# Kernel optimization log

Hardware: AMD Instinct MI355X
Metric: run time of the kernel (lower is better)

Reference implementation:

```python
import jax, jax.numpy as jnp
import numpy as np

N = 35709   # vertices
F = 70789   # triangles
B = 64
CAMERA_DISTANCE = 10.0
FOCAL = 1015.0
IMAGE_SIZE = 224

SH_A = (np.pi, 2 * np.pi / np.sqrt(3.0), 2 * np.pi / np.sqrt(8.0))
SH_C = (1 / np.sqrt(4 * np.pi), np.sqrt(3.0) / np.sqrt(4 * np.pi), 3 * np.sqrt(5.0) / np.sqrt(12 * np.pi))


def _persc_proj():
    center = IMAGE_SIZE / 2
    m = np.array([FOCAL, 0, center, 0, FOCAL, center, 0, 0, 1], dtype=np.float32).reshape(3, 3).T
    return jnp.asarray(m)


def setup_inputs() -> dict:
    key = jax.random.key(0)
    ks = jax.random.split(key, 9)
    return {
        "coeffs": jax.random.normal(ks[0], (B, 257), jnp.float32),
        "meanshape": jax.random.normal(ks[1], (3 * N,), jnp.float32),
        "idBase": jax.random.normal(ks[2], (3 * N, 80), jnp.float32),
        "exBase": jax.random.normal(ks[3], (3 * N, 64), jnp.float32),
        "meantex": jax.random.uniform(ks[4], (3 * N,), jnp.float32) * 255.0,
        "texBase": jax.random.normal(ks[5], (3 * N, 80), jnp.float32),
        "persc_proj": _persc_proj(),
        "init_lit": jnp.array([0.8, 0, 0, 0, 0, 0, 0, 0, 0], jnp.float32).reshape(1, 1, 9),
        "point_buf": jax.random.randint(ks[6], (N, 8), 0, F + 1),   # index F = zero-pad row
        "face_buf": jax.random.randint(ks[7], (F, 3), 0, N),
        "keypoints": jax.random.randint(ks[8], (68,), 0, N),
    }


def _l2norm(x):
    # matches torch F.normalize(p=2, eps=1e-12)
    return x / jnp.maximum(jnp.linalg.norm(x, axis=-1, keepdims=True), 1e-12)


def _rotation(angles):
    x, y, z = angles[:, 0], angles[:, 1], angles[:, 2]
    o, zr = jnp.ones_like(x), jnp.zeros_like(x)
    cx, sx = jnp.cos(x), jnp.sin(x)
    cy, sy = jnp.cos(y), jnp.sin(y)
    cz, sz = jnp.cos(z), jnp.sin(z)
    rx = jnp.stack([o, zr, zr, zr, cx, -sx, zr, sx, cx], -1).reshape(-1, 3, 3)
    ry = jnp.stack([cy, zr, sy, zr, o, zr, -sy, zr, cy], -1).reshape(-1, 3, 3)
    rz = jnp.stack([cz, -sz, zr, sz, cz, zr, zr, zr, o], -1).reshape(-1, 3, 3)
    return jnp.transpose(rz @ ry @ rx, (0, 2, 1))


def _compute_norm(face_shape, face_buf, point_buf):
    tri = face_shape[:, face_buf]                 # (B, F, 3verts, 3xyz) gather
    e1 = tri[:, :, 0] - tri[:, :, 1]
    e2 = tri[:, :, 1] - tri[:, :, 2]
    fn = _l2norm(jnp.cross(e1, e2))               # (B, F, 3)
    fn = jnp.concatenate([fn, jnp.zeros((fn.shape[0], 1, 3), fn.dtype)], axis=1)
    vn = jnp.sum(fn[:, point_buf], axis=2)        # (B, N, 3) gather-sum over 8 faces
    return _l2norm(vn)


def _compute_color(face_texture, face_norm, gamma, init_lit):
    a, c = SH_A, SH_C
    g = gamma.reshape(gamma.shape[0], 3, 9) + init_lit   # (B, 3, 9)
    g = jnp.transpose(g, (0, 2, 1))                      # (B, 9, 3)
    nx, ny, nz = face_norm[..., 0:1], face_norm[..., 1:2], face_norm[..., 2:3]
    Y = jnp.concatenate([
        a[0] * c[0] * jnp.ones_like(nx),
        -a[1] * c[1] * ny,
        a[1] * c[1] * nz,
        -a[1] * c[1] * nx,
        a[2] * c[2] * nx * ny,
        -a[2] * c[2] * ny * nz,
        0.5 * a[2] * c[2] / np.sqrt(3.0) * (3 * nz ** 2 - 1),
        -a[2] * c[2] * nx * nz,
        0.5 * a[2] * c[2] * (nx ** 2 - ny ** 2)], axis=-1)   # (B, N, 9)
    rgb = jnp.einsum('bnk,bkc->bnc', Y, g)
    return rgb * face_texture


def reference(coeffs, meanshape, idBase, exBase, meantex, texBase, persc_proj, init_lit, point_buf, face_buf, keypoints):
    id_c, ex_c, tex_c = coeffs[:, 0:80], coeffs[:, 80:144], coeffs[:, 144:224]
    angles, gamma, trans = coeffs[:, 224:227], coeffs[:, 227:254], coeffs[:, 254:257]
    Bsz = coeffs.shape[0]
    # shape blending (dense GEMMs)
    shape_flat = (jnp.einsum('ij,aj->ai', idBase, id_c)
                  + jnp.einsum('ij,aj->ai', exBase, ex_c)
                  + meanshape[None])
    face_shape = shape_flat.reshape(Bsz, -1, 3)
    rot = _rotation(angles)
    face_shape_t = face_shape @ rot + trans[:, None, :]
    # to camera: z -> camera_distance - z
    face_vertex = jnp.concatenate([face_shape_t[..., :2], CAMERA_DISTANCE - face_shape_t[..., 2:]], axis=-1)
    # perspective projection
    proj = face_vertex @ persc_proj
    face_proj = proj[..., :2] / proj[..., 2:]
    landmark = face_proj[:, keypoints, :]
    # texture blending
    face_texture = ((jnp.einsum('ij,aj->ai', texBase, tex_c) + meantex[None]) / 255.0).reshape(Bsz, -1, 3)
    # mesh normals on untransformed shape, rotated into camera frame
    face_norm = _compute_norm(face_shape, face_buf, point_buf)
    face_norm_r = face_norm @ rot
    face_color = _compute_color(face_texture, face_norm_r, gamma, init_lit)
    return face_vertex, face_color, landmark
```

## Files before the change

### kernel.cpp

```cpp
#include <hip/hip_runtime.h>

#define N_V 35709
#define N_F 70789
#define NR  (3*N_V)
#define NB  64

#define WS_ROT    0
#define WS_GM     576
#define WS_CTRS   2304
#define WS_CTRT   11520
#define WS_SHAPET 16640

__global__ __launch_bounds__(64) void k_setup_rot(
    const float* __restrict__ coeffs, const float* __restrict__ init_lit,
    float* __restrict__ rotM, float* __restrict__ gm)
{
    int b = threadIdx.x;
    const float* cb = coeffs + b * 257;

    float ax = cb[224], ay = cb[225], az = cb[226];
    float cx = cosf(ax), sx = sinf(ax);
    float cy = cosf(ay), sy = sinf(ay);
    float cz = cosf(az), sz = sinf(az);
    float m[9];
    m[0] = cz * cy;
    m[1] = cz * sy * sx - sz * cx;
    m[2] = sz * sx + cz * sy * cx;
    m[3] = sz * cy;
    m[4] = cz * cx + sz * sy * sx;
    m[5] = sz * sy * cx - cz * sx;
    m[6] = -sy;
    m[7] = cy * sx;
    m[8] = cy * cx;
#pragma unroll
    for (int k = 0; k < 9; k++) rotM[b * 9 + k] = m[k];

#pragma unroll
    for (int k = 0; k < 9; k++) {
        float il = init_lit[k];
#pragma unroll
        for (int c = 0; c < 3; c++)
            gm[b * 27 + k * 3 + c] = cb[227 + c * 9 + k] + il;
    }
}

__global__ __launch_bounds__(64) void k_transpose(
    const float* __restrict__ coeffs,
    float* __restrict__ ctrS, float* __restrict__ ctrT)
{
    int j = blockIdx.x;
    int b = threadIdx.x;
    float v = coeffs[b * 257 + j];
    if (j < 144) ctrS[j * 64 + b] = v;
    else         ctrT[(j - 144) * 64 + b] = v;
}

__global__ __launch_bounds__(256) void k_gemm_tile(
    const float* __restrict__ idBase, const float* __restrict__ exBase,
    const float* __restrict__ texBase, const float* __restrict__ meanshape,
    const float* __restrict__ meantex,
    const float* __restrict__ ctrS, const float* __restrict__ ctrT,
    float* __restrict__ shapeT,
    float* __restrict__ texT,
    int tex_transposed)
{
    __shared__ __align__(16) float As[16][68];
    __shared__ __align__(16) float Bs[16][64];

    const int t  = threadIdx.x;
    const int tn = t & 15;
    const int tm = t >> 4;
    const int r0 = blockIdx.x * 64;

    const int srow = t >> 2;
    const int sc   = t & 3;
    int srg = r0 + srow; if (srg > NR - 1) srg = NR - 1;

    float acc[4][4];

#pragma unroll
    for (int i = 0; i < 4; i++)
#pragma unroll
        for (int j = 0; j < 4; j++) acc[i][j] = 0.f;

    for (int kc = 0; kc < 9; kc++) {
        const float* src;
        int ld, k0;
        if (kc < 5) { src = idBase; ld = 80; k0 = kc * 16; }
        else        { src = exBase; ld = 64; k0 = (kc - 5) * 16; }

        {
            float4 v = *(const float4*)(src + (size_t)srg * ld + k0 + sc * 4);
            As[sc * 4 + 0][srow] = v.x;
            As[sc * 4 + 1][srow] = v.y;
            As[sc * 4 + 2][srow] = v.z;
            As[sc * 4 + 3][srow] = v.w;
        }
        ((float4*)&Bs[0][0])[t] = ((const float4*)(ctrS + (size_t)kc * 16 * 64))[t];
        __syncthreads();

#pragma unroll
        for (int k = 0; k < 16; k++) {
            float4 a = *(const float4*)&As[k][tm * 4];
            float4 b = *(const float4*)&Bs[k][tn * 4];
            float av[4] = {a.x, a.y, a.z, a.w};
            float bv[4] = {b.x, b.y, b.z, b.w};
#pragma unroll
            for (int i = 0; i < 4; i++)
#pragma unroll
                for (int j = 0; j < 4; j++)
                    acc[i][j] += av[i] * bv[j];
        }
        __syncthreads();
    }

#pragma unroll
    for (int i = 0; i < 4; i++) {
        int rg = r0 + tm * 4 + i;
        if (rg < NR) {
            float ms = meanshape[rg];
            float4 o = {acc[i][0] + ms, acc[i][1] + ms, acc[i][2] + ms, acc[i][3] + ms};
            *(float4*)(shapeT + (size_t)rg * 64 + tn * 4) = o;
        }
    }

#pragma unroll
    for (int i = 0; i < 4; i++)
#pragma unroll
        for (int j = 0; j < 4; j++) acc[i][j] = 0.f;

    for (int kc = 0; kc < 5; kc++) {
        int k0 = kc * 16;
        {
            float4 v = *(const float4*)(texBase + (size_t)srg * 80 + k0 + sc * 4);
            As[sc * 4 + 0][srow] = v.x;
            As[sc * 4 + 1][srow] = v.y;
            As[sc * 4 + 2][srow] = v.z;
            As[sc * 4 + 3][srow] = v.w;
        }
        ((float4*)&Bs[0][0])[t] = ((const float4*)(ctrT + (size_t)kc * 16 * 64))[t];
        __syncthreads();

#pragma unroll
        for (int k = 0; k < 16; k++) {
            float4 a = *(const float4*)&As[k][tm * 4];
            float4 b = *(const float4*)&Bs[k][tn * 4];
            float av[4] = {a.x, a.y, a.z, a.w};
            float bv[4] = {b.x, b.y, b.z, b.w};
#pragma unroll
            for (int i = 0; i < 4; i++)
#pragma unroll
                for (int j = 0; j < 4; j++)
                    acc[i][j] += av[i] * bv[j];
        }
        __syncthreads();
    }

    const float inv255 = 1.0f / 255.0f;
    if (tex_transposed) {
#pragma unroll
        for (int i = 0; i < 4; i++) {
            int rg = r0 + tm * 4 + i;
            if (rg < NR) {
                float mt = meantex[rg];
                float4 o = {(acc[i][0] + mt) * inv255, (acc[i][1] + mt) * inv255,
                            (acc[i][2] + mt) * inv255, (acc[i][3] + mt) * inv255};
                *(float4*)(texT + (size_t)rg * 64 + tn * 4) = o;
            }
        }
    } else {
#pragma unroll
        for (int i = 0; i < 4; i++) {
            int rg = r0 + tm * 4 + i;
            if (rg < NR) {
                float mt = meantex[rg];
#pragma unroll
                for (int j = 0; j < 4; j++)
                    texT[(size_t)(tn * 4 + j) * NR + rg] = (acc[i][j] + mt) * inv255;
            }
        }
    }
}

__global__ __launch_bounds__(256) void k_repack3(
    const float* __restrict__ shapeT, float* __restrict__ shape3)
{
    int wave = threadIdx.x >> 6;
    int b    = threadIdx.x & 63;
    int v0   = blockIdx.x * 32 + wave * 8;
#pragma unroll
    for (int r = 0; r < 8; r++) {
        int v = v0 + r;
        if (v < N_V) {
            float x = shapeT[(size_t)(3 * v)     * 64 + b];
            float y = shapeT[(size_t)(3 * v + 1) * 64 + b];
            float z = shapeT[(size_t)(3 * v + 2) * 64 + b];
            float* o = shape3 + ((size_t)v * 64 + b) * 3;
            o[0] = x; o[1] = y; o[2] = z;
        }
    }
}

__global__ __launch_bounds__(256) void k_facenorm3(
    const float* __restrict__ shape3,
    const int* __restrict__ face_buf,
    float* __restrict__ fnT3)
{
    int wave = threadIdx.x >> 6;
    int b    = threadIdx.x & 63;
    int f0   = blockIdx.x * 32 + wave * 8;
#pragma unroll
    for (int fr = 0; fr < 8; fr++) {
        int f = f0 + fr;
        if (f < N_F) {
            int i0 = face_buf[f * 3 + 0];
            int i1 = face_buf[f * 3 + 1];
            int i2 = face_buf[f * 3 + 2];
            const float* p0 = shape3 + ((size_t)i0 * 64 + b) * 3;
            const float* p1 = shape3 + ((size_t)i1 * 64 + b) * 3;
            const float* p2 = shape3 + ((size_t)i2 * 64 + b) * 3;
            float p0x = p0[0], p0y = p0[1], p0z = p0[2];
            float p1x = p1[0], p1y = p1[1], p1z = p1[2];
            float p2x = p2[0], p2y = p2[1], p2z = p2[2];
            float e1x = p0x - p1x, e1y = p0y - p1y, e1z = p0z - p1z;
            float e2x = p1x - p2x, e2y = p1y - p2y, e2z = p1z - p2z;
            float ccx = e1y * e2z - e1z * e2y;
            float ccy = e1z * e2x - e1x * e2z;
            float ccz = e1x * e2y - e1y * e2x;
            float l = sqrtf(ccx * ccx + ccy * ccy + ccz * ccz);
            float inv = 1.0f / fmaxf(l, 1e-12f);
            float* o = fnT3 + ((size_t)f * 64 + b) * 3;
            o[0] = ccx * inv; o[1] = ccy * inv; o[2] = ccz * inv;
        } else if (f == N_F) {
            float* o = fnT3 + ((size_t)f * 64 + b) * 3;
            o[0] = 0.f; o[1] = 0.f; o[2] = 0.f;
        }
    }
}

__global__ __launch_bounds__(256) void k_facenorm(
    const float* __restrict__ shapeT,
    const int* __restrict__ face_buf,
    float* __restrict__ fnT3)
{
    int wave = threadIdx.x >> 6;
    int b    = threadIdx.x & 63;
    int f0   = blockIdx.x * 32 + wave * 8;
#pragma unroll
    for (int fr = 0; fr < 8; fr++) {
        int f = f0 + fr;
        if (f < N_F) {
            int i0 = face_buf[f * 3 + 0];
            int i1 = face_buf[f * 3 + 1];
            int i2 = face_buf[f * 3 + 2];
            float p0x = shapeT[(size_t)(3 * i0)     * 64 + b];
            float p0y = shapeT[(size_t)(3 * i0 + 1) * 64 + b];
            float p0z = shapeT[(size_t)(3 * i0 + 2) * 64 + b];
            float p1x = shapeT[(size_t)(3 * i1)     * 64 + b];
            float p1y = shapeT[(size_t)(3 * i1 + 1) * 64 + b];
            float p1z = shapeT[(size_t)(3 * i1 + 2) * 64 + b];
            float p2x = shapeT[(size_t)(3 * i2)     * 64 + b];
            float p2y = shapeT[(size_t)(3 * i2 + 1) * 64 + b];
            float p2z = shapeT[(size_t)(3 * i2 + 2) * 64 + b];
            float e1x = p0x - p1x, e1y = p0y - p1y, e1z = p0z - p1z;
            float e2x = p1x - p2x, e2y = p1y - p2y, e2z = p1z - p2z;
            float ccx = e1y * e2z - e1z * e2y;
            float ccy = e1z * e2x - e1x * e2z;
            float ccz = e1x * e2y - e1y * e2x;
            float l = sqrtf(ccx * ccx + ccy * ccy + ccz * ccz);
            float inv = 1.0f / fmaxf(l, 1e-12f);
            float* o = fnT3 + ((size_t)f * 64 + b) * 3;
            o[0] = ccx * inv; o[1] = ccy * inv; o[2] = ccz * inv;
        } else if (f == N_F) {
            float* o = fnT3 + ((size_t)f * 64 + b) * 3;
            o[0] = 0.f; o[1] = 0.f; o[2] = 0.f;
        }
    }
}

__global__ __launch_bounds__(256) void k_vertex_fn(
    const float* __restrict__ shapeT,
    const float* __restrict__ texT,
    const float* __restrict__ fnT3,
    const float* __restrict__ rotM, const float* __restrict__ gm,
    const float* __restrict__ coeffs,
    const int* __restrict__ point_buf,
    float* __restrict__ out_vertex, float* __restrict__ out_color)
{
    __shared__ float sh[64 * 49];
    int wave = threadIdx.x >> 6;
    int b    = threadIdx.x & 63;
    int v0   = blockIdx.x * 16;
    int nvalid = N_V - v0; if (nvalid > 16) nvalid = 16;
    int kmax = 3 * nvalid;

    float m0 = rotM[b * 9 + 0], m1 = rotM[b * 9 + 1], m2 = rotM[b * 9 + 2];
    float m3 = rotM[b * 9 + 3], m4 = rotM[b * 9 + 4], m5 = rotM[b * 9 + 5];
    float m6 = rotM[b * 9 + 6], m7 = rotM[b * 9 + 7], m8 = rotM[b * 9 + 8];
    float tx = coeffs[b * 257 + 254], ty = coeffs[b * 257 + 255], tz = coeffs[b * 257 + 256];
    float g[27];
#pragma unroll
    for (int k = 0; k < 27; k++) g[k] = gm[b * 27 + k];

    const float A0C0 = 0.8862269254527580f;
    const float A1C1 = 1.7724538509055159f;
    const float A2C2 = 2.4270323912f;
    const float C6   = 0.7006239022f;
    const float C8   = 1.2135161956f;

    int pf[4][8];
    float sxv[4], syv[4], szv[4];
    float t0v[4], t1v[4], t2v[4];
#pragma unroll
    for (int vr = 0; vr < 4; vr++) {
        int v = v0 + wave * 4 + vr;
        int vc = (v < N_V) ? v : (N_V - 1);
#pragma unroll
        for (int k = 0; k < 8; k++) pf[vr][k] = point_buf[vc * 8 + k];
        sxv[vr] = shapeT[(size_t)(3 * vc)     * 64 + b];
        syv[vr] = shapeT[(size_t)(3 * vc + 1) * 64 + b];
        szv[vr] = shapeT[(size_t)(3 * vc + 2) * 64 + b];
        t0v[vr] = texT[(size_t)(3 * vc)     * 64 + b];
        t1v[vr] = texT[(size_t)(3 * vc + 1) * 64 + b];
        t2v[vr] = texT[(size_t)(3 * vc + 2) * 64 + b];
    }

    float vert[4][3];
    float col[4][3];

#pragma unroll
    for (int vr = 0; vr < 4; vr++) {
        float fx[8], fy[8], fz[8];
#pragma unroll
        for (int k = 0; k < 8; k++) {
            const float* fp = fnT3 + ((size_t)pf[vr][k] * 64 + b) * 3;
            fx[k] = fp[0]; fy[k] = fp[1]; fz[k] = fp[2];
        }

        float vx = m0 * sxv[vr] + m1 * syv[vr] + m2 * szv[vr] + tx;
        float vy = m3 * sxv[vr] + m4 * syv[vr] + m5 * szv[vr] + ty;
        float vz = m6 * sxv[vr] + m7 * syv[vr] + m8 * szv[vr] + tz;
        vert[vr][0] = vx; vert[vr][1] = vy; vert[vr][2] = 10.0f - vz;

        float nx = 0.f, ny = 0.f, nz = 0.f;
#pragma unroll
        for (int k = 0; k < 8; k++) { nx += fx[k]; ny += fy[k]; nz += fz[k]; }
        float l = sqrtf(nx * nx + ny * ny + nz * nz);
        float inv = 1.0f / fmaxf(l, 1e-12f);
        nx *= inv; ny *= inv; nz *= inv;

        float rx = m0 * nx + m1 * ny + m2 * nz;
        float ry = m3 * nx + m4 * ny + m5 * nz;
        float rz = m6 * nx + m7 * ny + m8 * nz;

        float Y0 = A0C0;
        float Y1 = -A1C1 * ry;
        float Y2 =  A1C1 * rz;
        float Y3 = -A1C1 * rx;
        float Y4 =  A2C2 * rx * ry;
        float Y5 = -A2C2 * ry * rz;
        float Y6 =  C6 * (3.f * rz * rz - 1.f);
        float Y7 = -A2C2 * rx * rz;
        float Y8 =  C8 * (rx * rx - ry * ry);

        float tex3[3] = {t0v[vr], t1v[vr], t2v[vr]};
#pragma unroll
        for (int c = 0; c < 3; c++) {
            float rgb = Y0 * g[0 + c] + Y1 * g[3 + c] + Y2 * g[6 + c] + Y3 * g[9 + c] +
                        Y4 * g[12 + c] + Y5 * g[15 + c] + Y6 * g[18 + c] + Y7 * g[21 + c] +
                        Y8 * g[24 + c];
            col[vr][c] = rgb * tex3[c];
        }
    }

#pragma unroll
    for (int vr = 0; vr < 4; vr++)
#pragma unroll
        for (int c = 0; c < 3; c++)
            sh[b * 49 + (wave * 4 + vr) * 3 + c] = vert[vr][c];
    __syncthreads();
#pragma unroll 4
    for (int it = 0; it < 12; it++) {
        int f = it * 256 + threadIdx.x;
        int bb = f / 48, k = f - bb * 48;
        if (k < kmax)
            __builtin_nontemporal_store(sh[bb * 49 + k],
                                        out_vertex + (size_t)bb * NR + 3 * (size_t)v0 + k);
    }
    __syncthreads();

#pragma unroll
    for (int vr = 0; vr < 4; vr++)
#pragma unroll
        for (int c = 0; c < 3; c++)
            sh[b * 49 + (wave * 4 + vr) * 3 + c] = col[vr][c];
    __syncthreads();
#pragma unroll 4
    for (int it = 0; it < 12; it++) {
        int f = it * 256 + threadIdx.x;
        int bb = f / 48, k = f - bb * 48;
        if (k < kmax)
            __builtin_nontemporal_store(sh[bb * 49 + k],
                                        out_color + (size_t)bb * NR + 3 * (size_t)v0 + k);
    }
}

__global__ __launch_bounds__(256) void k_vertex(
    const float* __restrict__ shapeT,
    const float* __restrict__ texT,
    const float* __restrict__ rotM, const float* __restrict__ gm,
    const float* __restrict__ coeffs,
    const int* __restrict__ point_buf, const int* __restrict__ face_buf,
    float* __restrict__ out_vertex, float* __restrict__ out_color,
    int tex_in_out)
{
    __shared__ float sh[64 * 97];
    int wave = threadIdx.x >> 6;
    int b    = threadIdx.x & 63;
    int v0   = blockIdx.x * 32;
    int nvalid = N_V - v0; if (nvalid > 32) nvalid = 32;
    int kmax = 3 * nvalid;

    float m0 = rotM[b * 9 + 0], m1 = rotM[b * 9 + 1], m2 = rotM[b * 9 + 2];
    float m3 = rotM[b * 9 + 3], m4 = rotM[b * 9 + 4], m5 = rotM[b * 9 + 5];
    float m6 = rotM[b * 9 + 6], m7 = rotM[b * 9 + 7], m8 = rotM[b * 9 + 8];
    float tx = coeffs[b * 257 + 254], ty = coeffs[b * 257 + 255], tz = coeffs[b * 257 + 256];
    float g[27];
#pragma unroll
    for (int k = 0; k < 27; k++) g[k] = gm[b * 27 + k];

    const float A0C0 = 0.8862269254527580f;
    const float A1C1 = 1.7724538509055159f;
    const float A2C2 = 2.4270323912f;
    const float C6   = 0.7006239022f;
    const float C8   = 1.2135161956f;

    float vert[8][3];
    float col[8][3];

#pragma unroll
    for (int vr = 0; vr < 8; vr++) {
        int v = v0 + wave * 8 + vr;
        bool valid = (v < N_V);
        int vc = valid ? v : (N_V - 1);

        float sx0 = shapeT[(size_t)(3 * vc)     * 64 + b];
        float sy0 = shapeT[(size_t)(3 * vc + 1) * 64 + b];
        float sz0 = shapeT[(size_t)(3 * vc + 2) * 64 + b];

        float vx = m0 * sx0 + m1 * sy0 + m2 * sz0 + tx;
        float vy = m3 * sx0 + m4 * sy0 + m5 * sz0 + ty;
        float vz = m6 * sx0 + m7 * sy0 + m8 * sz0 + tz;
        vert[vr][0] = vx; vert[vr][1] = vy; vert[vr][2] = 10.0f - vz;

        float nx = 0.f, ny = 0.f, nz = 0.f;
#pragma unroll
// ... 87 lines not shown
            __builtin_nontemporal_store(sh[bb * 97 + k],
                                        out_color + (size_t)bb * NR + 3 * (size_t)v0 + k);
    }
}

__global__ __launch_bounds__(64) void k_landmark(
    const float* __restrict__ shapeT, const int* __restrict__ keypoints,
    const float* __restrict__ rotM, const float* __restrict__ coeffs,
    const float* __restrict__ P,
    float* __restrict__ out_lm)
{
    int l = blockIdx.x;
    int b = threadIdx.x;
    int kp = keypoints[l];

    float m0 = rotM[b * 9 + 0], m1 = rotM[b * 9 + 1], m2 = rotM[b * 9 + 2];
    float m3 = rotM[b * 9 + 3], m4 = rotM[b * 9 + 4], m5 = rotM[b * 9 + 5];
    float m6 = rotM[b * 9 + 6], m7 = rotM[b * 9 + 7], m8 = rotM[b * 9 + 8];
    float tx = coeffs[b * 257 + 254], ty = coeffs[b * 257 + 255], tz = coeffs[b * 257 + 256];

    float sx0 = shapeT[(size_t)(3 * kp)     * 64 + b];
    float sy0 = shapeT[(size_t)(3 * kp + 1) * 64 + b];
    float sz0 = shapeT[(size_t)(3 * kp + 2) * 64 + b];

    float x = m0 * sx0 + m1 * sy0 + m2 * sz0 + tx;
    float y = m3 * sx0 + m4 * sy0 + m5 * sz0 + ty;
    float z = 10.0f - (m6 * sx0 + m7 * sy0 + m8 * sz0 + tz);

    float p0 = x * P[0] + y * P[3] + z * P[6];
    float p1 = x * P[1] + y * P[4] + z * P[7];
    float p2 = x * P[2] + y * P[5] + z * P[8];

    size_t o = ((size_t)b * 68 + l) * 2;
    out_lm[o]     = p0 / p2;
    out_lm[o + 1] = p1 / p2;
}

extern "C" void kernel_launch(void* const* d_in, const int* in_sizes, int n_in,
                              void* d_out, int out_size, void* d_ws, size_t ws_size,
                              hipStream_t stream) {
    const float* coeffs    = (const float*)d_in[0];
    const float* meanshape = (const float*)d_in[1];
    const float* idBase    = (const float*)d_in[2];
    const float* exBase    = (const float*)d_in[3];
    const float* meantex   = (const float*)d_in[4];
    const float* texBase   = (const float*)d_in[5];
    const float* persc     = (const float*)d_in[6];
    const float* init_lit  = (const float*)d_in[7];
    const int*   point_buf = (const int*)d_in[8];
    const int*   face_buf  = (const int*)d_in[9];
    const int*   keypoints = (const int*)d_in[10];

    float* ws = (float*)d_ws;
    float* rotM   = ws + WS_ROT;
    float* gm     = ws + WS_GM;
    float* ctrS   = ws + WS_CTRS;
    float* ctrT   = ws + WS_CTRT;
    float* shapeT = ws + WS_SHAPET;

    float* out_vertex = (float*)d_out;
    float* out_color  = out_vertex + (size_t)NB * NR;
    float* out_lm     = out_color  + (size_t)NB * NR;

    size_t NRx64   = (size_t)NR * 64;
    size_t fn3_len = (size_t)(N_F + 1) * 64 * 3;
    size_t sh3_len = (size_t)N_V * 64 * 3;

    size_t need_tex = ((size_t)WS_SHAPET + 2 * NRx64) * sizeof(float);
    size_t need_fn  = need_tex + fn3_len * sizeof(float);
    size_t need_s3  = need_fn + sh3_len * sizeof(float);

    int tex_transposed = (ws_size >= need_tex) ? 1 : 0;
    int use_fn         = (ws_size >= need_fn) ? 1 : 0;
    int use_s3         = (ws_size >= need_s3) ? 1 : 0;

    float* texT   = tex_transposed ? (shapeT + NRx64) : out_color;
    float* fnT3   = shapeT + 2 * NRx64;
    float* shape3 = fnT3 + fn3_len;

    k_setup_rot<<<1, 64, 0, stream>>>(coeffs, init_lit, rotM, gm);
    k_transpose<<<224, 64, 0, stream>>>(coeffs, ctrS, ctrT);

    int gb = (NR + 63) / 64;
    k_gemm_tile<<<gb, 256, 0, stream>>>(idBase, exBase, texBase, meanshape,
                                        meantex, ctrS, ctrT, shapeT, texT,
                                        tex_transposed);

    if (use_fn) {
        int fb = (N_F + 1 + 31) / 32;
        if (use_s3) {
            int rb = (N_V + 31) / 32;
            k_repack3<<<rb, 256, 0, stream>>>(shapeT, shape3);
            k_facenorm3<<<fb, 256, 0, stream>>>(shape3, face_buf, fnT3);
        } else {
            k_facenorm<<<fb, 256, 0, stream>>>(shapeT, face_buf, fnT3);
        }
        int vb = (N_V + 15) / 16;
        k_vertex_fn<<<vb, 256, 0, stream>>>(shapeT, texT, fnT3, rotM, gm, coeffs,
                                            point_buf, out_vertex, out_color);
    } else {
        int vb = (N_V + 31) / 32;
        k_vertex<<<vb, 256, 0, stream>>>(shapeT, tex_transposed ? texT : nullptr,
                                         rotM, gm, coeffs, point_buf, face_buf,
                                         out_vertex, out_color,
                                         tex_transposed ? 0 : 1);
    }

    k_landmark<<<68, 64, 0, stream>>>(shapeT, keypoints, rotM, coeffs, persc, out_lm);
}
```

Measured before the change: 278.6 us.

## Split shape/texture GEMMs, write vertex-major layout directly, co-schedule face normals

```diff
diff --git a/kernel.cpp b/kernel.cpp
--- a/kernel.cpp
+++ b/kernel.cpp
@@ -9,7 +9,7 @@
 #define WS_GM     576
 #define WS_CTRS   2304
 #define WS_CTRT   11520
-#define WS_SHAPET 16640
+#define WS_MAIN   16640
 
 __global__ __launch_bounds__(64) void k_setup_rot(
     const float* __restrict__ coeffs, const float* __restrict__ init_lit,
@@ -55,6 +55,332 @@
     else         ctrT[(j - 144) * 64 + b] = v;
 }
 
+__global__ __launch_bounds__(256) void k_gemm_shape3(
+    const float* __restrict__ idBase, const float* __restrict__ exBase,
+    const float* __restrict__ meanshape,
+    const float* __restrict__ ctrS,
+    float* __restrict__ shape3)
+{
+    __shared__ __align__(16) float As[16][68];
+    __shared__ __align__(16) float Bs[16][64];
+
+    const int t  = threadIdx.x;
+    const int tn = t & 15;
+    const int tm = t >> 4;
+    const int r0 = blockIdx.x * 64;
+
+    const int srow = t >> 2;
+    const int sc   = t & 3;
+    int srg = r0 + srow; if (srg > NR - 1) srg = NR - 1;
+
+    float acc[4][4];
+#pragma unroll
+    for (int i = 0; i < 4; i++)
+#pragma unroll
+        for (int j = 0; j < 4; j++) acc[i][j] = 0.f;
+
+    for (int kc = 0; kc < 9; kc++) {
+        const float* src;
+        int ld, k0;
+        if (kc < 5) { src = idBase; ld = 80; k0 = kc * 16; }
+        else        { src = exBase; ld = 64; k0 = (kc - 5) * 16; }
+
+        {
+            float4 v = *(const float4*)(src + (size_t)srg * ld + k0 + sc * 4);
+            As[sc * 4 + 0][srow] = v.x;
+            As[sc * 4 + 1][srow] = v.y;
+            As[sc * 4 + 2][srow] = v.z;
+            As[sc * 4 + 3][srow] = v.w;
+        }
+        ((float4*)&Bs[0][0])[t] = ((const float4*)(ctrS + (size_t)kc * 16 * 64))[t];
+        __syncthreads();
+
+#pragma unroll
+        for (int k = 0; k < 16; k++) {
+            float4 a = *(const float4*)&As[k][tm * 4];
+            float4 b = *(const float4*)&Bs[k][tn * 4];
+            float av[4] = {a.x, a.y, a.z, a.w};
+            float bv[4] = {b.x, b.y, b.z, b.w};
+#pragma unroll
+            for (int i = 0; i < 4; i++)
+#pragma unroll
+                for (int j = 0; j < 4; j++)
+                    acc[i][j] += av[i] * bv[j];
+        }
+        __syncthreads();
+    }
+
+#pragma unroll
+    for (int i = 0; i < 4; i++) {
+        int r = r0 + tm * 4 + i;
+        if (r < NR) {
+            float ms = meanshape[r];
+            int v = r / 3;
+            int c = r - v * 3;
+            float* o = shape3 + ((size_t)v * 64 + tn * 4) * 3 + c;
+            o[0] = acc[i][0] + ms;
+            o[3] = acc[i][1] + ms;
+            o[6] = acc[i][2] + ms;
+            o[9] = acc[i][3] + ms;
+        }
+    }
+}
+
+__global__ __launch_bounds__(256) void k_fn_texgemm(
+    const float* __restrict__ texBase, const float* __restrict__ meantex,
+    const float* __restrict__ ctrT,
+    const float* __restrict__ shape3, const int* __restrict__ face_buf,
+    float* __restrict__ tex3, float* __restrict__ fnT3, int GB)
+{
+    __shared__ __align__(16) float As[16][68];
+    __shared__ __align__(16) float Bs[16][64];
+
+    int x = blockIdx.x;
+    int role_tex, idx;
+    if (x < 2 * GB) { role_tex = ((x & 1) == 0); idx = x >> 1; }
+    else            { role_tex = 0; idx = x - GB; }
+
+    if (role_tex) {
+        const int t  = threadIdx.x;
+        const int tn = t & 15;
+        const int tm = t >> 4;
+        const int r0 = idx * 64;
+        const int srow = t >> 2;
+        const int sc   = t & 3;
+        int srg = r0 + srow; if (srg > NR - 1) srg = NR - 1;
+
+        float acc[4][4];
+#pragma unroll
+        for (int i = 0; i < 4; i++)
+#pragma unroll
+            for (int j = 0; j < 4; j++) acc[i][j] = 0.f;
+
+        for (int kc = 0; kc < 5; kc++) {
+            int k0 = kc * 16;
+            {
+                float4 v = *(const float4*)(texBase + (size_t)srg * 80 + k0 + sc * 4);
+                As[sc * 4 + 0][srow] = v.x;
+                As[sc * 4 + 1][srow] = v.y;
+                As[sc * 4 + 2][srow] = v.z;
+                As[sc * 4 + 3][srow] = v.w;
+            }
+            ((float4*)&Bs[0][0])[t] = ((const float4*)(ctrT + (size_t)kc * 16 * 64))[t];
+            __syncthreads();
+
+#pragma unroll
+            for (int k = 0; k < 16; k++) {
+                float4 a = *(const float4*)&As[k][tm * 4];
+                float4 b = *(const float4*)&Bs[k][tn * 4];
+                float av[4] = {a.x, a.y, a.z, a.w};
+                float bv[4] = {b.x, b.y, b.z, b.w};
+#pragma unroll
+                for (int i = 0; i < 4; i++)
+#pragma unroll
+                    for (int j = 0; j < 4; j++)
+                        acc[i][j] += av[i] * bv[j];
+            }
+            __syncthreads();
+        }
+
+        const float inv255 = 1.0f / 255.0f;
+#pragma unroll
+        for (int i = 0; i < 4; i++) {
+            int r = r0 + tm * 4 + i;
+            if (r < NR) {
+                float mt = meantex[r];
+                int v = r / 3;
+                int c = r - v * 3;
+                float* o = tex3 + ((size_t)v * 64 + tn * 4) * 3 + c;
+                o[0] = (acc[i][0] + mt) * inv255;
+                o[3] = (acc[i][1] + mt) * inv255;
+                o[6] = (acc[i][2] + mt) * inv255;
+                o[9] = (acc[i][3] + mt) * inv255;
+            }
+        }
+    } else {
+        int wave = threadIdx.x >> 6;
+        int b    = threadIdx.x & 63;
+        int f0   = idx * 32 + wave * 8;
+#pragma unroll
+        for (int fr = 0; fr < 8; fr++) {
+            int f = f0 + fr;
+            if (f < N_F) {
+                int i0 = face_buf[f * 3 + 0];
+                int i1 = face_buf[f * 3 + 1];
+                int i2 = face_buf[f * 3 + 2];
+                const float* p0 = shape3 + ((size_t)i0 * 64 + b) * 3;
+                const float* p1 = shape3 + ((size_t)i1 * 64 + b) * 3;
+                const float* p2 = shape3 + ((size_t)i2 * 64 + b) * 3;
+                float p0x = p0[0], p0y = p0[1], p0z = p0[2];
+                float p1x = p1[0], p1y = p1[1], p1z = p1[2];
+                float p2x = p2[0], p2y = p2[1], p2z = p2[2];
+                float e1x = p0x - p1x, e1y = p0y - p1y, e1z = p0z - p1z;
+                float e2x = p1x - p2x, e2y = p1y - p2y, e2z = p1z - p2z;
+                float ccx = e1y * e2z - e1z * e2y;
+                float ccy = e1z * e2x - e1x * e2z;
+                float ccz = e1x * e2y - e1y * e2x;
+                float l = sqrtf(ccx * ccx + ccy * ccy + ccz * ccz);
+                float inv = 1.0f / fmaxf(l, 1e-12f);
+                float* o = fnT3 + ((size_t)f * 64 + b) * 3;
+                o[0] = ccx * inv; o[1] = ccy * inv; o[2] = ccz * inv;
+            } else if (f == N_F) {
+                float* o = fnT3 + ((size_t)f * 64 + b) * 3;
+                o[0] = 0.f; o[1] = 0.f; o[2] = 0.f;
+            }
+        }
+    }
+}
+
+__global__ __launch_bounds__(256) void k_vertex_lm(
+    const float* __restrict__ shape3,
+    const float* __restrict__ tex3,
+    const float* __restrict__ fnT3,
+    const float* __restrict__ rotM, const float* __restrict__ gm,
+    const float* __restrict__ coeffs,
+    const int* __restrict__ point_buf, const int* __restrict__ keypoints,
+    const float* __restrict__ P,
+    float* __restrict__ out_vertex, float* __restrict__ out_color,
+    float* __restrict__ out_lm, int VB)
+{
+    __shared__ float sh[64 * 49];
+    int x    = blockIdx.x;
+    int wave = threadIdx.x >> 6;
+    int b    = threadIdx.x & 63;
+
+    float m0 = rotM[b * 9 + 0], m1 = rotM[b * 9 + 1], m2 = rotM[b * 9 + 2];
+    float m3 = rotM[b * 9 + 3], m4 = rotM[b * 9 + 4], m5 = rotM[b * 9 + 5];
+    float m6 = rotM[b * 9 + 6], m7 = rotM[b * 9 + 7], m8 = rotM[b * 9 + 8];
+    float tx = coeffs[b * 257 + 254], ty = coeffs[b * 257 + 255], tz = coeffs[b * 257 + 256];
+
+    if (x >= VB) {
+        int l = (x - VB) * 4 + wave;
+        if (l < 68) {
+            int kp = keypoints[l];
+            const float* sp = shape3 + ((size_t)kp * 64 + b) * 3;
+            float sx0 = sp[0], sy0 = sp[1], sz0 = sp[2];
+            float xx = m0 * sx0 + m1 * sy0 + m2 * sz0 + tx;
+            float yy = m3 * sx0 + m4 * sy0 + m5 * sz0 + ty;
+            float zz = 10.0f - (m6 * sx0 + m7 * sy0 + m8 * sz0 + tz);
+            float p0 = xx * P[0] + yy * P[3] + zz * P[6];
+            float p1 = xx * P[1] + yy * P[4] + zz * P[7];
+            float p2 = xx * P[2] + yy * P[5] + zz * P[8];
+            size_t o = ((size_t)b * 68 + l) * 2;
+            out_lm[o]     = p0 / p2;
+            out_lm[o + 1] = p1 / p2;
+        }
+        return;
+    }
+
+    int v0 = x * 16;
+    int nvalid = N_V - v0; if (nvalid > 16) nvalid = 16;
+    int kmax = 3 * nvalid;
+
+    float g[27];
+#pragma unroll
+    for (int k = 0; k < 27; k++) g[k] = gm[b * 27 + k];
+
+    const float A0C0 = 0.8862269254527580f;
+    const float A1C1 = 1.7724538509055159f;
+    const float A2C2 = 2.4270323912f;
+    const float C6   = 0.7006239022f;
+    const float C8   = 1.2135161956f;
+
+    int pf[4][8];
+    float sxv[4], syv[4], szv[4];
+    float t0v[4], t1v[4], t2v[4];
+#pragma unroll
+    for (int vr = 0; vr < 4; vr++) {
+        int v = v0 + wave * 4 + vr;
+        int vc = (v < N_V) ? v : (N_V - 1);
+#pragma unroll
+        for (int k = 0; k < 8; k++) pf[vr][k] = point_buf[vc * 8 + k];
+        const float* sp = shape3 + ((size_t)vc * 64 + b) * 3;
+        sxv[vr] = sp[0]; syv[vr] = sp[1]; szv[vr] = sp[2];
+        const float* tp = tex3 + ((size_t)vc * 64 + b) * 3;
+        t0v[vr] = tp[0]; t1v[vr] = tp[1]; t2v[vr] = tp[2];
+    }
+
+    float vert[4][3];
+    float col[4][3];
+
+#pragma unroll
+    for (int vr = 0; vr < 4; vr++) {
+        float fx[8], fy[8], fz[8];
+#pragma unroll
+        for (int k = 0; k < 8; k++) {
+            const float* fp = fnT3 + ((size_t)pf[vr][k] * 64 + b) * 3;
+            fx[k] = fp[0]; fy[k] = fp[1]; fz[k] = fp[2];
+        }
+
+        float vx = m0 * sxv[vr] + m1 * syv[vr] + m2 * szv[vr] + tx;
+        float vy = m3 * sxv[vr] + m4 * syv[vr] + m5 * szv[vr] + ty;
+        float vz = m6 * sxv[vr] + m7 * syv[vr] + m8 * szv[vr] + tz;
+        vert[vr][0] = vx; vert[vr][1] = vy; vert[vr][2] = 10.0f - vz;
+
+        float nx = 0.f, ny = 0.f, nz = 0.f;
+#pragma unroll
+        for (int k = 0; k < 8; k++) { nx += fx[k]; ny += fy[k]; nz += fz[k]; }
+        float l = sqrtf(nx * nx + ny * ny + nz * nz);
+        float inv = 1.0f / fmaxf(l, 1e-12f);
+        nx *= inv; ny *= inv; nz *= inv;
+
+        float rx = m0 * nx + m1 * ny + m2 * nz;
+        float ry = m3 * nx + m4 * ny + m5 * nz;
+        float rz = m6 * nx + m7 * ny + m8 * nz;
+
+        float Y0 = A0C0;
+        float Y1 = -A1C1 * ry;
+        float Y2 =  A1C1 * rz;
+        float Y3 = -A1C1 * rx;
+        float Y4 =  A2C2 * rx * ry;
+        float Y5 = -A2C2 * ry * rz;
+        float Y6 =  C6 * (3.f * rz * rz - 1.f);
+        float Y7 = -A2C2 * rx * rz;
+        float Y8 =  C8 * (rx * rx - ry * ry);
+
+        float tex3v[3] = {t0v[vr], t1v[vr], t2v[vr]};
+#pragma unroll
+        for (int c = 0; c < 3; c++) {
+            float rgb = Y0 * g[0 + c] + Y1 * g[3 + c] + Y2 * g[6 + c] + Y3 * g[9 + c] +
+                        Y4 * g[12 + c] + Y5 * g[15 + c] + Y6 * g[18 + c] + Y7 * g[21 + c] +
+                        Y8 * g[24 + c];
+            col[vr][c] = rgb * tex3v[c];
+        }
+    }
+
+#pragma unroll
+    for (int vr = 0; vr < 4; vr++)
+#pragma unroll
+        for (int c = 0; c < 3; c++)
+            sh[b * 49 + (wave * 4 + vr) * 3 + c] = vert[vr][c];
+    __syncthreads();
+#pragma unroll 4
+    for (int it = 0; it < 12; it++) {
+        int f = it * 256 + threadIdx.x;
+        int bb = f / 48, k = f - bb * 48;
+        if (k < kmax)
+            __builtin_nontemporal_store(sh[bb * 49 + k],
+                                        out_vertex + (size_t)bb * NR + 3 * (size_t)v0 + k);
+    }
+    __syncthreads();
+
+#pragma unroll
+    for (int vr = 0; vr < 4; vr++)
+#pragma unroll
+        for (int c = 0; c < 3; c++)
+            sh[b * 49 + (wave * 4 + vr) * 3 + c] = col[vr][c];
+    __syncthreads();
+#pragma unroll 4
+    for (int it = 0; it < 12; it++) {
+        int f = it * 256 + threadIdx.x;
+        int bb = f / 48, k = f - bb * 48;
+        if (k < kmax)
+            __builtin_nontemporal_store(sh[bb * 49 + k],
+                                        out_color + (size_t)bb * NR + 3 * (size_t)v0 + k);
+    }
+}
+
+
 __global__ __launch_bounds__(256) void k_gemm_tile(
     const float* __restrict__ idBase, const float* __restrict__ exBase,
     const float* __restrict__ texBase, const float* __restrict__ meanshape,
@@ -77,7 +403,6 @@
     int srg = r0 + srow; if (srg > NR - 1) srg = NR - 1;
 
     float acc[4][4];
-
 #pragma unroll
     for (int i = 0; i < 4; i++)
 #pragma unroll
@@ -88,7 +413,6 @@
         int ld, k0;
         if (kc < 5) { src = idBase; ld = 80; k0 = kc * 16; }
         else        { src = exBase; ld = 64; k0 = (kc - 5) * 16; }
-
         {
             float4 v = *(const float4*)(src + (size_t)srg * ld + k0 + sc * 4);
             As[sc * 4 + 0][srow] = v.x;
@@ -98,7 +422,6 @@
         }
         ((float4*)&Bs[0][0])[t] = ((const float4*)(ctrS + (size_t)kc * 16 * 64))[t];
         __syncthreads();
-
 #pragma unroll
         for (int k = 0; k < 16; k++) {
             float4 a = *(const float4*)&As[k][tm * 4];
@@ -140,7 +463,6 @@
         }
         ((float4*)&Bs[0][0])[t] = ((const float4*)(ctrT + (size_t)kc * 16 * 64))[t];
         __syncthreads();
-
 #pragma unroll
         for (int k = 0; k < 16; k++) {
             float4 a = *(const float4*)&As[k][tm * 4];
@@ -179,229 +501,6 @@
                     texT[(size_t)(tn * 4 + j) * NR + rg] = (acc[i][j] + mt) * inv255;
             }
         }
-    }
-}
-
-__global__ __launch_bounds__(256) void k_repack3(
-    const float* __restrict__ shapeT, float* __restrict__ shape3)
-{
-    int wave = threadIdx.x >> 6;
-    int b    = threadIdx.x & 63;
-    int v0   = blockIdx.x * 32 + wave * 8;
-#pragma unroll
-    for (int r = 0; r < 8; r++) {
-        int v = v0 + r;
-        if (v < N_V) {
-            float x = shapeT[(size_t)(3 * v)     * 64 + b];
-            float y = shapeT[(size_t)(3 * v + 1) * 64 + b];
-            float z = shapeT[(size_t)(3 * v + 2) * 64 + b];
-            float* o = shape3 + ((size_t)v * 64 + b) * 3;
-            o[0] = x; o[1] = y; o[2] = z;
-        }
-    }
-}
-
-__global__ __launch_bounds__(256) void k_facenorm3(
-    const float* __restrict__ shape3,
-    const int* __restrict__ face_buf,
-    float* __restrict__ fnT3)
-{
-    int wave = threadIdx.x >> 6;
-    int b    = threadIdx.x & 63;
-    int f0   = blockIdx.x * 32 + wave * 8;
-#pragma unroll
-    for (int fr = 0; fr < 8; fr++) {
-        int f = f0 + fr;
-        if (f < N_F) {
-            int i0 = face_buf[f * 3 + 0];
-            int i1 = face_buf[f * 3 + 1];
-            int i2 = face_buf[f * 3 + 2];
-            const float* p0 = shape3 + ((size_t)i0 * 64 + b) * 3;
-            const float* p1 = shape3 + ((size_t)i1 * 64 + b) * 3;
-            const float* p2 = shape3 + ((size_t)i2 * 64 + b) * 3;
-            float p0x = p0[0], p0y = p0[1], p0z = p0[2];
-            float p1x = p1[0], p1y = p1[1], p1z = p1[2];
-            float p2x = p2[0], p2y = p2[1], p2z = p2[2];
-            float e1x = p0x - p1x, e1y = p0y - p1y, e1z = p0z - p1z;
-            float e2x = p1x - p2x, e2y = p1y - p2y, e2z = p1z - p2z;
-            float ccx = e1y * e2z - e1z * e2y;
-            float ccy = e1z * e2x - e1x * e2z;
-            float ccz = e1x * e2y - e1y * e2x;
-            float l = sqrtf(ccx * ccx + ccy * ccy + ccz * ccz);
-            float inv = 1.0f / fmaxf(l, 1e-12f);
-            float* o = fnT3 + ((size_t)f * 64 + b) * 3;
-            o[0] = ccx * inv; o[1] = ccy * inv; o[2] = ccz * inv;
-        } else if (f == N_F) {
-            float* o = fnT3 + ((size_t)f * 64 + b) * 3;
-            o[0] = 0.f; o[1] = 0.f; o[2] = 0.f;
-        }
-    }
-}
-
-__global__ __launch_bounds__(256) void k_facenorm(
-    const float* __restrict__ shapeT,
-    const int* __restrict__ face_buf,
-    float* __restrict__ fnT3)
-{
-    int wave = threadIdx.x >> 6;
-    int b    = threadIdx.x & 63;
-    int f0   = blockIdx.x * 32 + wave * 8;
-#pragma unroll
-    for (int fr = 0; fr < 8; fr++) {
-        int f = f0 + fr;
-        if (f < N_F) {
-            int i0 = face_buf[f * 3 + 0];
-            int i1 = face_buf[f * 3 + 1];
-            int i2 = face_buf[f * 3 + 2];
-            float p0x = shapeT[(size_t)(3 * i0)     * 64 + b];
-            float p0y = shapeT[(size_t)(3 * i0 + 1) * 64 + b];
-            float p0z = shapeT[(size_t)(3 * i0 + 2) * 64 + b];
-            float p1x = shapeT[(size_t)(3 * i1)     * 64 + b];
-            float p1y = shapeT[(size_t)(3 * i1 + 1) * 64 + b];
-            float p1z = shapeT[(size_t)(3 * i1 + 2) * 64 + b];
-            float p2x = shapeT[(size_t)(3 * i2)     * 64 + b];
-            float p2y = shapeT[(size_t)(3 * i2 + 1) * 64 + b];
-            float p2z = shapeT[(size_t)(3 * i2 + 2) * 64 + b];
-            float e1x = p0x - p1x, e1y = p0y - p1y, e1z = p0z - p1z;
-            float e2x = p1x - p2x, e2y = p1y - p2y, e2z = p1z - p2z;
-            float ccx = e1y * e2z - e1z * e2y;
-            float ccy = e1z * e2x - e1x * e2z;
-            float ccz = e1x * e2y - e1y * e2x;
-            float l = sqrtf(ccx * ccx + ccy * ccy + ccz * ccz);
-            float inv = 1.0f / fmaxf(l, 1e-12f);
-            float* o = fnT3 + ((size_t)f * 64 + b) * 3;
-            o[0] = ccx * inv; o[1] = ccy * inv; o[2] = ccz * inv;
-        } else if (f == N_F) {
-            float* o = fnT3 + ((size_t)f * 64 + b) * 3;
-            o[0] = 0.f; o[1] = 0.f; o[2] = 0.f;
-        }
-    }
-}
-
-__global__ __launch_bounds__(256) void k_vertex_fn(
-    const float* __restrict__ shapeT,
-    const float* __restrict__ texT,
-    const float* __restrict__ fnT3,
-    const float* __restrict__ rotM, const float* __restrict__ gm,
-    const float* __restrict__ coeffs,
-    const int* __restrict__ point_buf,
-    float* __restrict__ out_vertex, float* __restrict__ out_color)
-{
-    __shared__ float sh[64 * 49];
-    int wave = threadIdx.x >> 6;
-    int b    = threadIdx.x & 63;
-    int v0   = blockIdx.x * 16;
-    int nvalid = N_V - v0; if (nvalid > 16) nvalid = 16;
-    int kmax = 3 * nvalid;
-
-    float m0 = rotM[b * 9 + 0], m1 = rotM[b * 9 + 1], m2 = rotM[b * 9 + 2];
-    float m3 = rotM[b * 9 + 3], m4 = rotM[b * 9 + 4], m5 = rotM[b * 9 + 5];
-    float m6 = rotM[b * 9 + 6], m7 = rotM[b * 9 + 7], m8 = rotM[b * 9 + 8];
-    float tx = coeffs[b * 257 + 254], ty = coeffs[b * 257 + 255], tz = coeffs[b * 257 + 256];
-    float g[27];
-#pragma unroll
-    for (int k = 0; k < 27; k++) g[k] = gm[b * 27 + k];
-
-    const float A0C0 = 0.8862269254527580f;
-    const float A1C1 = 1.7724538509055159f;
-    const float A2C2 = 2.4270323912f;
-    const float C6   = 0.7006239022f;
-    const float C8   = 1.2135161956f;
-
-    int pf[4][8];
-    float sxv[4], syv[4], szv[4];
-    float t0v[4], t1v[4], t2v[4];
-#pragma unroll
-    for (int vr = 0; vr < 4; vr++) {
-        int v = v0 + wave * 4 + vr;
-        int vc = (v < N_V) ? v : (N_V - 1);
-#pragma unroll
-        for (int k = 0; k < 8; k++) pf[vr][k] = point_buf[vc * 8 + k];
-        sxv[vr] = shapeT[(size_t)(3 * vc)     * 64 + b];
-        syv[vr] = shapeT[(size_t)(3 * vc + 1) * 64 + b];
-        szv[vr] = shapeT[(size_t)(3 * vc + 2) * 64 + b];
-        t0v[vr] = texT[(size_t)(3 * vc)     * 64 + b];
-        t1v[vr] = texT[(size_t)(3 * vc + 1) * 64 + b];
-        t2v[vr] = texT[(size_t)(3 * vc + 2) * 64 + b];
-    }
-
-    float vert[4][3];
-    float col[4][3];
-
-#pragma unroll
-    for (int vr = 0; vr < 4; vr++) {
-        float fx[8], fy[8], fz[8];
-#pragma unroll
-        for (int k = 0; k < 8; k++) {
-            const float* fp = fnT3 + ((size_t)pf[vr][k] * 64 + b) * 3;
-            fx[k] = fp[0]; fy[k] = fp[1]; fz[k] = fp[2];
-        }
-
-        float vx = m0 * sxv[vr] + m1 * syv[vr] + m2 * szv[vr] + tx;
-        float vy = m3 * sxv[vr] + m4 * syv[vr] + m5 * szv[vr] + ty;
-        float vz = m6 * sxv[vr] + m7 * syv[vr] + m8 * szv[vr] + tz;
-        vert[vr][0] = vx; vert[vr][1] = vy; vert[vr][2] = 10.0f - vz;
-
-        float nx = 0.f, ny = 0.f, nz = 0.f;
-#pragma unroll
-        for (int k = 0; k < 8; k++) { nx += fx[k]; ny += fy[k]; nz += fz[k]; }
-        float l = sqrtf(nx * nx + ny * ny + nz * nz);
-        float inv = 1.0f / fmaxf(l, 1e-12f);
-        nx *= inv; ny *= inv; nz *= inv;
-
-        float rx = m0 * nx + m1 * ny + m2 * nz;
-        float ry = m3 * nx + m4 * ny + m5 * nz;
-        float rz = m6 * nx + m7 * ny + m8 * nz;
-
-        float Y0 = A0C0;
-        float Y1 = -A1C1 * ry;
-        float Y2 =  A1C1 * rz;
-        float Y3 = -A1C1 * rx;
-        float Y4 =  A2C2 * rx * ry;
-        float Y5 = -A2C2 * ry * rz;
-        float Y6 =  C6 * (3.f * rz * rz - 1.f);
-        float Y7 = -A2C2 * rx * rz;
-        float Y8 =  C8 * (rx * rx - ry * ry);
-
-        float tex3[3] = {t0v[vr], t1v[vr], t2v[vr]};
-#pragma unroll
-        for (int c = 0; c < 3; c++) {
-            float rgb = Y0 * g[0 + c] + Y1 * g[3 + c] + Y2 * g[6 + c] + Y3 * g[9 + c] +
-                        Y4 * g[12 + c] + Y5 * g[15 + c] + Y6 * g[18 + c] + Y7 * g[21 + c] +
-                        Y8 * g[24 + c];
-            col[vr][c] = rgb * tex3[c];
-        }
-    }
-
-#pragma unroll
-    for (int vr = 0; vr < 4; vr++)
-#pragma unroll
-        for (int c = 0; c < 3; c++)
-            sh[b * 49 + (wave * 4 + vr) * 3 + c] = vert[vr][c];
-    __syncthreads();
-#pragma unroll 4
-    for (int it = 0; it < 12; it++) {
-        int f = it * 256 + threadIdx.x;
-        int bb = f / 48, k = f - bb * 48;
-        if (k < kmax)
-            __builtin_nontemporal_store(sh[bb * 49 + k],
-                                        out_vertex + (size_t)bb * NR + 3 * (size_t)v0 + k);
-    }
-    __syncthreads();
-
-#pragma unroll
-    for (int vr = 0; vr < 4; vr++)
-#pragma unroll
-        for (int c = 0; c < 3; c++)
-            sh[b * 49 + (wave * 4 + vr) * 3 + c] = col[vr][c];
-    __syncthreads();
-#pragma unroll 4
-    for (int it = 0; it < 12; it++) {
-        int f = it * 256 + threadIdx.x;
-        int bb = f / 48, k = f - bb * 48;
-        if (k < kmax)
-            __builtin_nontemporal_store(sh[bb * 49 + k],
-                                        out_color + (size_t)bb * NR + 3 * (size_t)v0 + k);
     }
 }
 
@@ -595,59 +694,55 @@
     const int*   keypoints = (const int*)d_in[10];
 
     float* ws = (float*)d_ws;
-    float* rotM   = ws + WS_ROT;
-    float* gm     = ws + WS_GM;
-    float* ctrS   = ws + WS_CTRS;
-    float* ctrT   = ws + WS_CTRT;
-    float* shapeT = ws + WS_SHAPET;
+    float* rotM = ws + WS_ROT;
+    float* gm   = ws + WS_GM;
+    float* ctrS = ws + WS_CTRS;
+    float* ctrT = ws + WS_CTRT;
 
     float* out_vertex = (float*)d_out;
     float* out_color  = out_vertex + (size_t)NB * NR;
     float* out_lm     = out_color  + (size_t)NB * NR;
 
-    size_t NRx64   = (size_t)NR * 64;
+    size_t sh3_len = (size_t)N_V * 64 * 3;
     size_t fn3_len = (size_t)(N_F + 1) * 64 * 3;
-    size_t sh3_len = (size_t)N_V * 64 * 3;
-
-    size_t need_tex = ((size_t)WS_SHAPET + 2 * NRx64) * sizeof(float);
-    size_t need_fn  = need_tex + fn3_len * sizeof(float);
-    size_t need_s3  = need_fn + sh3_len * sizeof(float);
-
-    int tex_transposed = (ws_size >= need_tex) ? 1 : 0;
-    int use_fn         = (ws_size >= need_fn) ? 1 : 0;
-    int use_s3         = (ws_size >= need_s3) ? 1 : 0;
-
-    float* texT   = tex_transposed ? (shapeT + NRx64) : out_color;
-    float* fnT3   = shapeT + 2 * NRx64;
-    float* shape3 = fnT3 + fn3_len;
+
+    size_t need_new = ((size_t)WS_MAIN + 2 * sh3_len + fn3_len) * sizeof(float);
+    size_t need_tex = ((size_t)WS_MAIN + 2 * sh3_len) * sizeof(float);
 
     k_setup_rot<<<1, 64, 0, stream>>>(coeffs, init_lit, rotM, gm);
     k_transpose<<<224, 64, 0, stream>>>(coeffs, ctrS, ctrT);
 
-    int gb = (NR + 63) / 64;
-    k_gemm_tile<<<gb, 256, 0, stream>>>(idBase, exBase, texBase, meanshape,
-                                        meantex, ctrS, ctrT, shapeT, texT,
-                                        tex_transposed);
-
-    if (use_fn) {
-        int fb = (N_F + 1 + 31) / 32;
-        if (use_s3) {
-            int rb = (N_V + 31) / 32;
-            k_repack3<<<rb, 256, 0, stream>>>(shapeT, shape3);
-            k_facenorm3<<<fb, 256, 0, stream>>>(shape3, face_buf, fnT3);
-        } else {
-            k_facenorm<<<fb, 256, 0, stream>>>(shapeT, face_buf, fnT3);
-        }
-        int vb = (N_V + 15) / 16;
-        k_vertex_fn<<<vb, 256, 0, stream>>>(shapeT, texT, fnT3, rotM, gm, coeffs,
-                                            point_buf, out_vertex, out_color);
+    const int GB = (NR + 63) / 64;
+
+    if (ws_size >= need_new) {
+        float* shape3 = ws + WS_MAIN;
+        float* tex3   = shape3 + sh3_len;
+        float* fnT3   = tex3 + sh3_len;
+
+        k_gemm_shape3<<<GB, 256, 0, stream>>>(idBase, exBase, meanshape, ctrS, shape3);
+
+        const int FB = (N_F + 1 + 31) / 32;
+        k_fn_texgemm<<<GB + FB, 256, 0, stream>>>(texBase, meantex, ctrT,
+                                                  shape3, face_buf, tex3, fnT3, GB);
+
+        const int VB = (N_V + 15) / 16;
+        const int LB = (68 + 3) / 4;
+        k_vertex_lm<<<VB + LB, 256, 0, stream>>>(shape3, tex3, fnT3, rotM, gm,
+                                                 coeffs, point_buf, keypoints, persc,
+                                                 out_vertex, out_color, out_lm, VB);
     } else {
+        int tex_transposed = (ws_size >= need_tex) ? 1 : 0;
+        float* shapeT = ws + WS_MAIN;
+        float* texT   = tex_transposed ? (shapeT + sh3_len) : out_color;
+
+        k_gemm_tile<<<GB, 256, 0, stream>>>(idBase, exBase, texBase, meanshape,
+                                            meantex, ctrS, ctrT, shapeT, texT,
+                                            tex_transposed);
         int vb = (N_V + 31) / 32;
         k_vertex<<<vb, 256, 0, stream>>>(shapeT, tex_transposed ? texT : nullptr,
                                          rotM, gm, coeffs, point_buf, face_buf,
                                          out_vertex, out_color,
                                          tex_transposed ? 0 : 1);
-    }
-
-    k_landmark<<<68, 64, 0, stream>>>(shapeT, keypoints, rotM, coeffs, persc, out_lm);
-}
+        k_landmark<<<68, 64, 0, stream>>>(shapeT, keypoints, rotM, coeffs, persc, out_lm);
+    }
+}
```

Measured after the change: 299.6 us. +7.5%, slower.

## Double-buffer GEMM smem tiles and fuse shape3 repack into GEMM epilogue

Applied to the files above, without the earlier changes.

```diff
diff --git a/kernel.cpp b/kernel.cpp
--- a/kernel.cpp
+++ b/kernel.cpp
@@ -62,10 +62,11 @@
     const float* __restrict__ ctrS, const float* __restrict__ ctrT,
     float* __restrict__ shapeT,
     float* __restrict__ texT,
-    int tex_transposed)
-{
-    __shared__ __align__(16) float As[16][68];
-    __shared__ __align__(16) float Bs[16][64];
+    float* __restrict__ shape3,
+    int write_s3, int tex_transposed)
+{
+    __shared__ __align__(16) float As[2][16][68];
+    __shared__ __align__(16) float Bs[2][16][64];
 
     const int t  = threadIdx.x;
     const int tn = t & 15;
@@ -83,26 +84,34 @@
 #pragma unroll
         for (int j = 0; j < 4; j++) acc[i][j] = 0.f;
 
+    {
+        float4 v = *(const float4*)(idBase + (size_t)srg * 80 + sc * 4);
+        As[0][sc * 4 + 0][srow] = v.x;
+        As[0][sc * 4 + 1][srow] = v.y;
+        As[0][sc * 4 + 2][srow] = v.z;
+        As[0][sc * 4 + 3][srow] = v.w;
+        ((float4*)&Bs[0][0][0])[t] = ((const float4*)ctrS)[t];
+    }
+    __syncthreads();
+
     for (int kc = 0; kc < 9; kc++) {
-        const float* src;
-        int ld, k0;
-        if (kc < 5) { src = idBase; ld = 80; k0 = kc * 16; }
-        else        { src = exBase; ld = 64; k0 = (kc - 5) * 16; }
-
-        {
-            float4 v = *(const float4*)(src + (size_t)srg * ld + k0 + sc * 4);
-            As[sc * 4 + 0][srow] = v.x;
-            As[sc * 4 + 1][srow] = v.y;
-            As[sc * 4 + 2][srow] = v.z;
-            As[sc * 4 + 3][srow] = v.w;
-        }
-        ((float4*)&Bs[0][0])[t] = ((const float4*)(ctrS + (size_t)kc * 16 * 64))[t];
-        __syncthreads();
+        const int cur = kc & 1;
+        const int nxt = cur ^ 1;
+        float4 pa, pb;
+        const bool havenext = (kc + 1 < 9);
+        if (havenext) {
+            const float* src;
+            int ld, k0;
+            if (kc + 1 < 5) { src = idBase; ld = 80; k0 = (kc + 1) * 16; }
+            else            { src = exBase; ld = 64; k0 = (kc + 1 - 5) * 16; }
+            pa = *(const float4*)(src + (size_t)srg * ld + k0 + sc * 4);
+            pb = ((const float4*)(ctrS + (size_t)(kc + 1) * 16 * 64))[t];
+        }
 
 #pragma unroll
         for (int k = 0; k < 16; k++) {
-            float4 a = *(const float4*)&As[k][tm * 4];
-            float4 b = *(const float4*)&Bs[k][tn * 4];
+            float4 a = *(const float4*)&As[cur][k][tm * 4];
+            float4 b = *(const float4*)&Bs[cur][k][tn * 4];
             float av[4] = {a.x, a.y, a.z, a.w};
             float bv[4] = {b.x, b.y, b.z, b.w};
 #pragma unroll
@@ -110,6 +119,14 @@
 #pragma unroll
                 for (int j = 0; j < 4; j++)
                     acc[i][j] += av[i] * bv[j];
+        }
+
+        if (havenext) {
+            As[nxt][sc * 4 + 0][srow] = pa.x;
+            As[nxt][sc * 4 + 1][srow] = pa.y;
+            As[nxt][sc * 4 + 2][srow] = pa.z;
+            As[nxt][sc * 4 + 3][srow] = pa.w;
+            ((float4*)&Bs[nxt][0][0])[t] = pb;
         }
         __syncthreads();
     }
@@ -119,8 +136,16 @@
         int rg = r0 + tm * 4 + i;
         if (rg < NR) {
             float ms = meanshape[rg];
-            float4 o = {acc[i][0] + ms, acc[i][1] + ms, acc[i][2] + ms, acc[i][3] + ms};
+            float s0 = acc[i][0] + ms, s1 = acc[i][1] + ms;
+            float s2 = acc[i][2] + ms, s3 = acc[i][3] + ms;
+            float4 o = {s0, s1, s2, s3};
             *(float4*)(shapeT + (size_t)rg * 64 + tn * 4) = o;
+            if (write_s3) {
+                int v = rg / 3;
+                int c = rg - v * 3;
+                float* p = shape3 + ((size_t)v * 64 + tn * 4) * 3 + c;
+                p[0] = s0; p[3] = s1; p[6] = s2; p[9] = s3;
+            }
         }
     }
 
@@ -129,22 +154,31 @@
 #pragma unroll
         for (int j = 0; j < 4; j++) acc[i][j] = 0.f;
 
+    {
+        float4 v = *(const float4*)(texBase + (size_t)srg * 80 + sc * 4);
+        As[0][sc * 4 + 0][srow] = v.x;
+        As[0][sc * 4 + 1][srow] = v.y;
+        As[0][sc * 4 + 2][srow] = v.z;
+        As[0][sc * 4 + 3][srow] = v.w;
+        ((float4*)&Bs[0][0][0])[t] = ((const float4*)ctrT)[t];
+    }
+    __syncthreads();
+
     for (int kc = 0; kc < 5; kc++) {
-        int k0 = kc * 16;
-        {
-            float4 v = *(const float4*)(texBase + (size_t)srg * 80 + k0 + sc * 4);
-            As[sc * 4 + 0][srow] = v.x;
-            As[sc * 4 + 1][srow] = v.y;
-            As[sc * 4 + 2][srow] = v.z;
-            As[sc * 4 + 3][srow] = v.w;
-        }
-        ((float4*)&Bs[0][0])[t] = ((const float4*)(ctrT + (size_t)kc * 16 * 64))[t];
-        __syncthreads();
+        const int cur = kc & 1;
+        const int nxt = cur ^ 1;
+        float4 pa, pb;
+        const bool havenext = (kc + 1 < 5);
+        if (havenext) {
+            int k0 = (kc + 1) * 16;
+            pa = *(const float4*)(texBase + (size_t)srg * 80 + k0 + sc * 4);
+            pb = ((const float4*)(ctrT + (size_t)(kc + 1) * 16 * 64))[t];
+        }
 
 #pragma unroll
         for (int k = 0; k < 16; k++) {
-            float4 a = *(const float4*)&As[k][tm * 4];
-            float4 b = *(const float4*)&Bs[k][tn * 4];
+            float4 a = *(const float4*)&As[cur][k][tm * 4];
+            float4 b = *(const float4*)&Bs[cur][k][tn * 4];
             float av[4] = {a.x, a.y, a.z, a.w};
             float bv[4] = {b.x, b.y, b.z, b.w};
 #pragma unroll
@@ -152,6 +186,14 @@
 #pragma unroll
                 for (int j = 0; j < 4; j++)
                     acc[i][j] += av[i] * bv[j];
+        }
+
+        if (havenext) {
+            As[nxt][sc * 4 + 0][srow] = pa.x;
+            As[nxt][sc * 4 + 1][srow] = pa.y;
+            As[nxt][sc * 4 + 2][srow] = pa.z;
+            As[nxt][sc * 4 + 3][srow] = pa.w;
+            ((float4*)&Bs[nxt][0][0])[t] = pb;
         }
         __syncthreads();
     }
@@ -178,25 +220,6 @@
                 for (int j = 0; j < 4; j++)
                     texT[(size_t)(tn * 4 + j) * NR + rg] = (acc[i][j] + mt) * inv255;
             }
-        }
-    }
-}
-
-__global__ __launch_bounds__(256) void k_repack3(
-    const float* __restrict__ shapeT, float* __restrict__ shape3)
-{
-    int wave = threadIdx.x >> 6;
-    int b    = threadIdx.x & 63;
-    int v0   = blockIdx.x * 32 + wave * 8;
-#pragma unroll
-    for (int r = 0; r < 8; r++) {
-        int v = v0 + r;
-        if (v < N_V) {
-            float x = shapeT[(size_t)(3 * v)     * 64 + b];
-            float y = shapeT[(size_t)(3 * v + 1) * 64 + b];
-            float z = shapeT[(size_t)(3 * v + 2) * 64 + b];
-            float* o = shape3 + ((size_t)v * 64 + b) * 3;
-            o[0] = x; o[1] = y; o[2] = z;
         }
     }
 }
@@ -595,10 +618,10 @@
     const int*   keypoints = (const int*)d_in[10];
 
     float* ws = (float*)d_ws;
-    float* rotM   = ws + WS_ROT;
-    float* gm     = ws + WS_GM;
-    float* ctrS   = ws + WS_CTRS;
-    float* ctrT   = ws + WS_CTRT;
+    float* rotM = ws + WS_ROT;
+    float* gm   = ws + WS_GM;
+    float* ctrS = ws + WS_CTRS;
+    float* ctrT = ws + WS_CTRT;
     float* shapeT = ws + WS_SHAPET;
 
     float* out_vertex = (float*)d_out;
@@ -627,13 +650,11 @@
     int gb = (NR + 63) / 64;
     k_gemm_tile<<<gb, 256, 0, stream>>>(idBase, exBase, texBase, meanshape,
                                         meantex, ctrS, ctrT, shapeT, texT,
-                                        tex_transposed);
+                                        shape3, use_s3, tex_transposed);
 
     if (use_fn) {
         int fb = (N_F + 1 + 31) / 32;
         if (use_s3) {
-            int rb = (N_V + 31) / 32;
-            k_repack3<<<rb, 256, 0, stream>>>(shapeT, shape3);
             k_facenorm3<<<fb, 256, 0, stream>>>(shape3, face_buf, fnT3);
         } else {
             k_facenorm<<<fb, 256, 0, stream>>>(shapeT, face_buf, fnT3);
```

New measurement: 287.6 us. 1.03x slower.
